# Performance work log

Hardware: AMD Instinct MI355X
Metric: run time of the kernel (lower is better)

## Reference

```python
import jax, jax.numpy as jnp
import numpy as np

B, S, D, H = 4, 4096, 1024, 16
DK = D // H
EPS = 1e-6

def _feature_map(x):
    # ELU + 1 -> strictly positive features
    return jax.nn.elu(x) + 1.0

def setup_inputs() -> dict:
    key = jax.random.key(0)
    ks = jax.random.split(key, 11)
    s = 1.0 / np.sqrt(D)
    return {
        "query": jax.random.normal(ks[0], (B, S, D), jnp.float32),
        "key":   jax.random.normal(ks[1], (B, S, D), jnp.float32),
        "value": jax.random.normal(ks[2], (B, S, D), jnp.float32),
        "Wq": jax.random.uniform(ks[3], (D, D), jnp.float32, -s, s),
        "bq": jax.random.uniform(ks[4], (D,), jnp.float32, -s, s),
        "Wk": jax.random.uniform(ks[5], (D, D), jnp.float32, -s, s),
        "bk": jax.random.uniform(ks[6], (D,), jnp.float32, -s, s),
        "Wv": jax.random.uniform(ks[7], (D, D), jnp.float32, -s, s),
        "bv": jax.random.uniform(ks[8], (D,), jnp.float32, -s, s),
        "Wo": jax.random.uniform(ks[9], (D, D), jnp.float32, -s, s),
        "bo": jax.random.uniform(ks[10], (D,), jnp.float32, -s, s),
    }

def reference(query, key, value, Wq, bq, Wk, bk, Wv, bv, Wo, bo):
    def heads(x, W, b):
        # torch Linear: x @ W.T + b, then split heads -> [B, H, S, DK]
        y = x @ W.T + b
        return y.reshape(B, S, H, DK).transpose(0, 2, 1, 3)

    Q = _feature_map(heads(query, Wq, bq))
    K = _feature_map(heads(key, Wk, bk))
    V = heads(value, Wv, bv)

    # KV[b,h,m,d] = sum_n K[b,h,n,d] * V[b,h,n,m]  (d: K feat dim, m: V dim)
    KV = jnp.einsum('bhnd,bhnm->bhmd', K, V)
    # normalizer Z[b,h,n] = Q[b,h,n,:] . sum_n K
    Z = jnp.einsum('bhnd,bhd->bhn', Q, K.sum(axis=2))[..., None] + EPS
    out = jnp.einsum('bhnd,bhmd->bhnm', Q, KV) / Z  # [B,H,S,DK]
    out = out.transpose(0, 2, 1, 3).reshape(B, S, D)
    return out @ Wo.T + bo
```

## Files before the change

kernel.cpp:

```cpp
#include <hip/hip_runtime.h>
#include <math.h>

#define Bb 4
#define Ss 4096
#define Dd 1024
#define Hh 16
#define DKk 64
#define Mm (Bb * Ss)
#define NCH 16

typedef __attribute__((ext_vector_type(8))) short bf16x8;
typedef __attribute__((ext_vector_type(4))) float f32x4;

__device__ __forceinline__ unsigned short f2bf(float f) {
  unsigned u = __float_as_uint(f);
  u += 0x7FFFu + ((u >> 16) & 1u);
  return (unsigned short)(u >> 16);
}
__device__ __forceinline__ float bf2f(unsigned short s) {
  return __uint_as_float(((unsigned)s) << 16);
}
__device__ __forceinline__ unsigned cvt2(float lo, float hi) {
  unsigned r;
  asm("v_cvt_pk_bf16_f32 %0, %1, %2" : "=v"(r) : "v"(lo), "v"(hi));
  return r;
}
__device__ __forceinline__ void cvt8(const float* __restrict__ s,
                                     unsigned short* __restrict__ d, long i) {
  float4 a = ((const float4*)s)[2 * i];
  float4 b = ((const float4*)s)[2 * i + 1];
  int4 w;
  w.x = cvt2(a.x, a.y); w.y = cvt2(a.z, a.w);
  w.z = cvt2(b.x, b.y); w.w = cvt2(b.z, b.w);
  ((int4*)d)[i] = w;
}

#define GLOAD(dst, src)                                                     \
  __builtin_amdgcn_global_load_lds(                                         \
      (const __attribute__((address_space(1))) void*)(src),                 \
      (__attribute__((address_space(3))) void*)(dst), 16, 0, 0)

__global__ __launch_bounds__(256) void cvt_all(
    const float* __restrict__ k, const float* __restrict__ v,
    const float* __restrict__ Wq, const float* __restrict__ Wk,
    const float* __restrict__ Wv, const float* __restrict__ Wo,
    unsigned short* __restrict__ kb, unsigned short* __restrict__ vb,
    unsigned short* __restrict__ Wqb, unsigned short* __restrict__ Wkb,
    unsigned short* __restrict__ Wvb, unsigned short* __restrict__ Wob) {
  const int z = blockIdx.z;
  if (z < 2) {
    const float* s = z ? v : k;
    unsigned short* d = z ? vb : kb;
    const long n8 = ((long)Mm * Dd) / 8;
    for (long i = (long)blockIdx.x * 256 + threadIdx.x; i < n8;
         i += (long)gridDim.x * 256)
      cvt8(s, d, i);
  } else {
    const long n8w = ((long)Dd * Dd) / 8;
    for (long i = (long)blockIdx.x * 256 + threadIdx.x; i < 4 * n8w;
         i += (long)gridDim.x * 256) {
      const int which = (int)(i / n8w);
      const long off = i - (long)which * n8w;
      const float* s = (which == 0) ? Wq : (which == 1) ? Wk
                       : (which == 2) ? Wv : Wo;
      unsigned short* d = (which == 0) ? Wqb : (which == 1) ? Wkb
                          : (which == 2) ? Wvb : Wob;
      cvt8(s, d, off);
    }
  }
}

#define LOADA2(dst, mh)                                                      \
  _Pragma("unroll") for (int mi = 0; mi < 4; ++mi)                           \
    _Pragma("unroll") for (int ks = 0; ks < 2; ++ks)                         \
      dst[mi][ks] = *(const bf16x8*)(bufA +                                  \
          ((mh) * 128 + wm * 64 + mi * 16 + fr) * 64 + (swz_rd ^ (ks * 32)));

#define LOADB2(dst, nh)                                                      \
  _Pragma("unroll") for (int ni = 0; ni < 2; ++ni)                           \
    _Pragma("unroll") for (int ks = 0; ks < 2; ++ks)                         \
      dst[ni][ks] = *(const bf16x8*)(bufB +                                  \
          ((nh) * 128 + wn * 32 + ni * 16 + fr) * 64 + (swz_rd ^ (ks * 32)));

#define MFMAQ2(a_, b_, mh, nh)                                               \
  __builtin_amdgcn_s_setprio(1);                                             \
  _Pragma("unroll") for (int mi = 0; mi < 4; ++mi)                           \
    _Pragma("unroll") for (int ni = 0; ni < 2; ++ni)                         \
      _Pragma("unroll") for (int ks = 0; ks < 2; ++ks)                       \
        acc[(mh) * 4 + mi][(nh) * 2 + ni] =                                  \
            __builtin_amdgcn_mfma_f32_16x16x32_bf16(                         \
                a_[mi][ks], b_[ni][ks],                                      \
                acc[(mh) * 4 + mi][(nh) * 2 + ni], 0, 0, 0);                 \
  __builtin_amdgcn_s_setprio(0);

template <typename OutT>
__device__ __forceinline__ void gemm256_body(
    const unsigned short* __restrict__ A,
    const unsigned short* __restrict__ W,
    const float* __restrict__ bias,
    OutT* __restrict__ C, const int act, const int wg_in,
    unsigned short* lds) {
  const int t = threadIdx.x;
  const int wave = t >> 6, lane = t & 63;
  const int wm = wave >> 2, wn = wave & 3;
  const int fr = lane & 15, fq = lane >> 4;

  const int wg = ((wg_in & 7) << 5) | (wg_in >> 3);
  const int bm = wg >> 2, bn = wg & 3;

  f32x4 acc[8][4];
#pragma unroll
  for (int i = 0; i < 8; ++i)
#pragma unroll
    for (int j = 0; j < 4; ++j) acc[i][j] = (f32x4){0.f, 0.f, 0.f, 0.f};

  const int r = t >> 3;
  const int swz_st = ((t & 7) ^ (r & 7)) << 3;
  const unsigned short* gA[4];
  const unsigned short* gB[4];
#pragma unroll
  for (int l = 0; l < 4; ++l) {
    const int ga_row = (l & 1) * 128 + (l >> 1) * 64 + r;
    const int bb = l * 2 + (r >> 5);
    const int gb_row = (bb & 3) * 64 + (bb >> 2) * 32 + (r & 31);
    gA[l] = A + (size_t)(bm * 256 + ga_row) * Dd + swz_st;
    gB[l] = W + (size_t)(bn * 256 + gb_row) * Dd + swz_st;
  }
  const int dstoff = wave * 512;

  const int swz_rd = (fq * 8) ^ ((fr & 7) << 3);

  GLOAD(lds + 0 * 4096 + dstoff, gA[0]);
  GLOAD(lds + 1 * 4096 + dstoff, gA[1]);
  GLOAD(lds + 16384 + 0 * 4096 + dstoff, gB[0]);
  GLOAD(lds + 16384 + 1 * 4096 + dstoff, gB[1]);
  GLOAD(lds + 2 * 4096 + dstoff, gA[2]);
  GLOAD(lds + 3 * 4096 + dstoff, gA[3]);
  GLOAD(lds + 16384 + 2 * 4096 + dstoff, gB[2]);
  GLOAD(lds + 16384 + 3 * 4096 + dstoff, gB[3]);
  asm volatile("s_waitcnt vmcnt(4)" ::: "memory");
  __builtin_amdgcn_s_barrier();

  for (int tt = 0; tt < 16; ++tt) {
    unsigned short* bufA = lds + (tt & 1) * 32768;
    unsigned short* bufB = bufA + 16384;
    unsigned short* nA = lds + ((tt & 1) ^ 1) * 32768;
    unsigned short* nB = nA + 16384;
    const int kpre = (tt < 15 ? tt + 1 : 15) * 64;

    bf16x8 afr0[4][2], afr1[4][2], bvr0[2][2], bvr1[2][2];
    LOADA2(afr0, 0)
    LOADB2(bvr0, 0)
    GLOAD(nA + 0 * 4096 + dstoff, gA[0] + kpre);
    GLOAD(nA + 1 * 4096 + dstoff, gA[1] + kpre);
    GLOAD(nB + 0 * 4096 + dstoff, gB[0] + kpre);
    GLOAD(nB + 1 * 4096 + dstoff, gB[1] + kpre);
    asm volatile("s_waitcnt vmcnt(4)" ::: "memory");
    __builtin_amdgcn_s_barrier();
    MFMAQ2(afr0, bvr0, 0, 0)
    LOADB2(bvr1, 1)
    GLOAD(nA + 2 * 4096 + dstoff, gA[2] + kpre);
    GLOAD(nA + 3 * 4096 + dstoff, gA[3] + kpre);
    GLOAD(nB + 2 * 4096 + dstoff, gB[2] + kpre);
    GLOAD(nB + 3 * 4096 + dstoff, gB[3] + kpre);
    MFMAQ2(afr0, bvr1, 0, 1)
    LOADA2(afr1, 1)
    MFMAQ2(afr1, bvr1, 1, 1)
    MFMAQ2(afr1, bvr0, 1, 0)
    asm volatile("s_waitcnt vmcnt(4) lgkmcnt(0)" ::: "memory");
    __builtin_amdgcn_s_barrier();
  }

  const size_t row0 = (size_t)bm * 256 + wm * 128 + fq * 4;
  const int col0 = bn * 256 + wn * 64 + fr;
#pragma unroll
  for (int a = 0; a < 8; ++a) {
    const size_t row_a = row0 + (a >> 2) * 64 + (a & 3) * 16;
#pragma unroll
    for (int b = 0; b < 4; ++b) {
      const int col = col0 + (b >> 1) * 32 + (b & 1) * 16;
      const float bvl = bias[col];
#pragma unroll
      for (int rr2 = 0; rr2 < 4; ++rr2) {
        const size_t row = row_a + rr2;
        float vv = acc[a][b][rr2] + bvl;
        if (act) vv = (vv > 0.f) ? (vv + 1.f) : __expf(vv);
        if constexpr (sizeof(OutT) == 2)
          ((unsigned short*)C)[row * Dd + col] = f2bf(vv);
        else
          ((float*)C)[row * Dd + col] = vv;
      }
    }
  }
}

template <int ACT, typename OutT>
__global__ __launch_bounds__(512, 2) void gemm256(
    const unsigned short* __restrict__ A, const unsigned short* __restrict__ W,
    const float* __restrict__ bias, OutT* __restrict__ C) {
  __shared__ __align__(16) unsigned short lds[2 * 32768];
  gemm256_body<OutT>(A, W, bias, C, ACT,
                     blockIdx.x + gridDim.x * blockIdx.y, lds);
}

__global__ __launch_bounds__(512, 2) void gemm256_kv(
    const unsigned short* __restrict__ A0, const unsigned short* __restrict__ W0,
    const float* __restrict__ b0, unsigned short* __restrict__ C0,
    const unsigned short* __restrict__ A1, const unsigned short* __restrict__ W1,
    const float* __restrict__ b1, unsigned short* __restrict__ C1) {
  __shared__ __align__(16) unsigned short lds[2 * 32768];
  const int wg = blockIdx.x + gridDim.x * blockIdx.y;
  if (blockIdx.z == 0)
    gemm256_body<unsigned short>(A0, W0, b0, C0, 1, wg, lds);
  else
    gemm256_body<unsigned short>(A1, W1, b1, C1, 0, wg, lds);
}

__global__ __launch_bounds__(512, 2) void gemm256_qred(
    const unsigned short* __restrict__ A, const unsigned short* __restrict__ W,
    const float* __restrict__ bias, unsigned short* __restrict__ C,
    const float* __restrict__ part, float* __restrict__ KV,
    float* __restrict__ Ksum) {
  __shared__ __align__(16) unsigned short lds[2 * 32768];
  const int wg = blockIdx.x + gridDim.x * blockIdx.y;
  if (blockIdx.z == 0) {
    gemm256_body<unsigned short>(A, W, bias, C, 1, wg, lds);
  } else {
    const int bh = wg;
    if (bh >= Bb * Hh || threadIdx.x >= 256) return;
    for (int e = threadIdx.x; e < 4160; e += 256) {
      float s = 0.f;
#pragma unroll
      for (int c = 0; c < NCH; ++c)
        s += part[((size_t)bh * NCH + c) * 4160 + e];
      if (e < 4096) KV[(size_t)bh * 4096 + e] = s;
      else Ksum[bh * 64 + (e - 4096)] = s;
    }
  }
}

__global__ __launch_bounds__(256) void kvp_cvtq(
    const unsigned short* __restrict__ Kf, const unsigned short* __restrict__ Vf,
    float* __restrict__ part,
    const float* __restrict__ q, unsigned short* __restrict__ qb) {
  if (blockIdx.y == 1) {
    const long n8 = ((long)Mm * Dd) / 8;
    for (long i = (long)blockIdx.x * 256 + threadIdx.x; i < n8;
         i += (long)gridDim.x * 256)
      cvt8(q, qb, i);
    return;
  }
  const int bx = blockIdx.x;
  if (bx >= Bb * Hh * NCH) return;
  const int chunk = bx % NCH;
  const int bh = bx / NCH;
  const int h = bh % Hh, b = bh / Hh;
  const int t = threadIdx.x;
  const int tm = t >> 4, td = t & 15;
  __shared__ float sK[8][64];
  __shared__ float sV[8][64];
  float acc[4][4] = {{0.f}};
  float ksr[4] = {0.f, 0.f, 0.f, 0.f};

  const int which = t >> 7;
  const int idx = t & 127;
  const int rr = idx >> 4;
  const int dpos = (idx & 15) << 2;
  const int colbase = h * DKk;
  const int rows = Ss / NCH;

  for (int n0 = 0; n0 < rows; n0 += 8) {
    const int gr = b * Ss + chunk * rows + n0 + rr;
    const unsigned short* src = which ? Vf : Kf;
    ushort4 raw = *(const ushort4*)&src[(size_t)gr * Dd + colbase + dpos];
    __syncthreads();
    float* dst = which ? &sV[rr][dpos] : &sK[rr][dpos];
    dst[0] = bf2f(raw.x); dst[1] = bf2f(raw.y);
    dst[2] = bf2f(raw.z); dst[3] = bf2f(raw.w);
    __syncthreads();
#pragma unroll
    for (int r = 0; r < 8; ++r) {
      float kv[4], vv[4];
#pragma unroll
      for (int j = 0; j < 4; ++j) kv[j] = sK[r][td * 4 + j];
#pragma unroll
      for (int i = 0; i < 4; ++i) vv[i] = sV[r][tm * 4 + i];
#pragma unroll
      for (int i = 0; i < 4; ++i)
#pragma unroll
        for (int j = 0; j < 4; ++j)
          acc[i][j] = fmaf(vv[i], kv[j], acc[i][j]);
      if (tm == 0) {
#pragma unroll
        for (int j = 0; j < 4; ++j) ksr[j] += kv[j];
      }
    }
  }

  float* p = part + (size_t)bx * 4160;
#pragma unroll
  for (int i = 0; i < 4; ++i)
#pragma unroll
    for (int j = 0; j < 4; ++j)
      p[(tm * 4 + i) * 64 + td * 4 + j] = acc[i][j];
  if (tm == 0) {
#pragma unroll
    for (int j = 0; j < 4; ++j) p[4096 + td * 4 + j] = ksr[j];
  }
}

__global__ __launch_bounds__(256) void attn_mfma(
    unsigned short* __restrict__ Qf, const float* __restrict__ KV,
    const float* __restrict__ Ksum) {
  const int bh = blockIdx.x;
  const int h = bh & (Hh - 1), b = bh >> 4;
  const int t = threadIdx.x;
  const int wave = t >> 6, lane = t & 63;
  const int fr = lane & 15, fq = lane >> 4;

  bf16x8 bfrag[4][2];
  const float* kvb = KV + (size_t)bh * 4096;
#pragma unroll
  for (int nj = 0; nj < 4; ++nj)
#pragma unroll
    for (int ks = 0; ks < 2; ++ks) {
      const float* src = kvb + (nj * 16 + fr) * 64 + ks * 32 + fq * 8;
      const float4 lo = *(const float4*)src;
      const float4 hi = *(const float4*)(src + 4);
      bf16x8 f;
      f[0] = (short)f2bf(lo.x); f[1] = (short)f2bf(lo.y);
      f[2] = (short)f2bf(lo.z); f[3] = (short)f2bf(lo.w);
      f[4] = (short)f2bf(hi.x); f[5] = (short)f2bf(hi.y);
      f[6] = (short)f2bf(hi.z); f[7] = (short)f2bf(hi.w);
      bfrag[nj][ks] = f;
    }
  bf16x8 zfrag[2];
#pragma unroll
  for (int ks = 0; ks < 2; ++ks) {
    bf16x8 f = (bf16x8){0, 0, 0, 0, 0, 0, 0, 0};
    if (fr == 0) {
      const float* src = Ksum + bh * 64 + ks * 32 + fq * 8;
      const float4 lo = *(const float4*)src;
      const float4 hi = *(const float4*)(src + 4);
      f[0] = (short)f2bf(lo.x); f[1] = (short)f2bf(lo.y);
      f[2] = (short)f2bf(lo.z); f[3] = (short)f2bf(lo.w);
      f[4] = (short)f2bf(hi.x); f[5] = (short)f2bf(hi.y);
      f[6] = (short)f2bf(hi.z); f[7] = (short)f2bf(hi.w);
    }
    zfrag[ks] = f;
  }

  const size_t row0 = (size_t)b * Ss + (size_t)blockIdx.y * 256 + wave * 64;
  unsigned short* qbase = Qf + row0 * Dd + h * DKk;
  bf16x8 afrag[4][2];
#pragma unroll
  for (int mi = 0; mi < 4; ++mi)
#pragma unroll
    for (int ks = 0; ks < 2; ++ks)
      afrag[mi][ks] =
          *(const bf16x8*)(qbase + (size_t)(mi * 16 + fr) * Dd + ks * 32 + fq * 8);

  f32x4 acc[4][4], zacc[4];
#pragma unroll
  for (int mi = 0; mi < 4; ++mi) {
    zacc[mi] = (f32x4){0.f, 0.f, 0.f, 0.f};
#pragma unroll
    for (int nj = 0; nj < 4; ++nj) acc[mi][nj] = (f32x4){0.f, 0.f, 0.f, 0.f};
  }
#pragma unroll
  for (int mi = 0; mi < 4; ++mi)
#pragma unroll
    for (int ks = 0; ks < 2; ++ks) {
      zacc[mi] = __builtin_amdgcn_mfma_f32_16x16x32_bf16(
          afrag[mi][ks], zfrag[ks], zacc[mi], 0, 0, 0);
#pragma unroll
      for (int nj = 0; nj < 4; ++nj)
        acc[mi][nj] = __builtin_amdgcn_mfma_f32_16x16x32_bf16(
            afrag[mi][ks], bfrag[nj][ks], acc[mi][nj], 0, 0, 0);
    }

#pragma unroll
  for (int mi = 0; mi < 4; ++mi)
#pragma unroll
    for (int r = 0; r < 4; ++r) {
      const float zv = __shfl(zacc[mi][r], lane & 48) + 1e-6f;
      const float rz = 1.0f / zv;
      const size_t ro = (size_t)(mi * 16 + fq * 4 + r) * Dd;
#pragma unroll
      for (int nj = 0; nj < 4; ++nj)
        qbase[ro + nj * 16 + fr] = f2bf(acc[mi][nj][r] * rz);
    }
}

extern "C" void kernel_launch(void* const* d_in, const int* in_sizes, int n_in,
                              void* d_out, int out_size, void* d_ws, size_t ws_size,
                              hipStream_t stream) {
  const float* q  = (const float*)d_in[0];
  const float* k  = (const float*)d_in[1];
  const float* v  = (const float*)d_in[2];
  const float* Wq = (const float*)d_in[3];
  const float* bq = (const float*)d_in[4];
  const float* Wk = (const float*)d_in[5];
  const float* bk = (const float*)d_in[6];
  const float* Wv = (const float*)d_in[7];
  const float* bv = (const float*)d_in[8];
  const float* Wo = (const float*)d_in[9];
  const float* bo = (const float*)d_in[10];
  float* out = (float*)d_out;

  unsigned short* kb  = (unsigned short*)d_ws;
  unsigned short* vb  = kb + (size_t)Mm * Dd;
  unsigned short* Kf  = vb + (size_t)Mm * Dd;
  unsigned short* Vf  = Kf + (size_t)Mm * Dd;
  unsigned short* Wqb = Vf + (size_t)Mm * Dd;
  unsigned short* Wkb = Wqb + (size_t)Dd * Dd;
  unsigned short* Wvb = Wkb + (size_t)Dd * Dd;
  unsigned short* Wob = Wvb + (size_t)Dd * Dd;
  float* KV   = (float*)(Wob + (size_t)Dd * Dd);
  float* Ksum = KV + (size_t)Bb * Hh * DKk * DKk;
  float* part = (float*)vb;

  dim3 gg(Dd / 256, Mm / 256);
  dim3 ggz(Dd / 256, Mm / 256, 2);

  cvt_all<<<dim3(2048, 1, 3), 256, 0, stream>>>(k, v, Wq, Wk, Wv, Wo,
                                                kb, vb, Wqb, Wkb, Wvb, Wob);
  gemm256_kv<<<ggz, 512, 0, stream>>>(kb, Wkb, bk, Kf, vb, Wvb, bv, Vf);
  kvp_cvtq<<<dim3(2048, 2), 256, 0, stream>>>(Kf, Vf, part, q, kb);
  gemm256_qred<<<ggz, 512, 0, stream>>>(kb, Wqb, bq, Kf, part, KV, Ksum);
  attn_mfma<<<dim3(Bb * Hh, Ss / 256), 256, 0, stream>>>(Kf, KV, Ksum);
  gemm256<0, float><<<gg, 512, 0, stream>>>(Kf, Wob, bo, out);
  (void)in_sizes; (void)n_in; (void)out_size; (void)ws_size;
}
```

Measured before the change: 262.9 us.

## Load weight fragments directly from global memory into registers, skipping LDS staging

The GEMM body now reads the B operand (weight rows) straight from global memory into MFMA register fragments instead of staging it through LDS, and prefetches the next K-step's B fragment one tile ahead. The loop is unrolled by two so two fragment buffers can ping-pong. LDS use is halved to A tiles only, which lowers LDS traffic and may allow more occupancy. In exchange, each wave issues uncoalesced 16-byte global loads for its weight rows, and the same weight data is fetched redundantly by every wave with the same wn, relying on L2/L1 hits.

```diff
diff --git a/kernel.cpp b/kernel.cpp
--- a/kernel.cpp
+++ b/kernel.cpp
@@ -76,11 +76,11 @@
       dst[mi][ks] = *(const bf16x8*)(bufA +                                  \
           ((mh) * 128 + wm * 64 + mi * 16 + fr) * 64 + (swz_rd ^ (ks * 32)));
 
-#define LOADB2(dst, nh)                                                      \
+#define BLOAD(dst, nh, tt)                                                   \
   _Pragma("unroll") for (int ni = 0; ni < 2; ++ni)                           \
     _Pragma("unroll") for (int ks = 0; ks < 2; ++ks)                         \
-      dst[ni][ks] = *(const bf16x8*)(bufB +                                  \
-          ((nh) * 128 + wn * 32 + ni * 16 + fr) * 64 + (swz_rd ^ (ks * 32)));
+      dst[ni][ks] = *(const bf16x8*)(Wp +                                    \
+          (size_t)((nh) * 32 + ni * 16) * Dd + (tt) * 64 + ks * 32);
 
 #define MFMAQ2(a_, b_, mh, nh)                                               \
   __builtin_amdgcn_s_setprio(1);                                             \
@@ -92,6 +92,29 @@
                 a_[mi][ks], b_[ni][ks],                                      \
                 acc[(mh) * 4 + mi][(nh) * 2 + ni], 0, 0, 0);                 \
   __builtin_amdgcn_s_setprio(0);
+
+#define TILEBODY(tt, B0C, B0N)                                               \
+  {                                                                          \
+    const int kpre = ((tt) < 15 ? (tt) + 1 : 15) * 64;                       \
+    unsigned short* bufA = lds + ((tt) & 1) * 16384;                         \
+    unsigned short* nA = lds + ((((tt) & 1)) ^ 1) * 16384;                   \
+    bf16x8 afr0[4][2], afr1[4][2], B1[2][2];                                 \
+    BLOAD(B1, 1, tt)                                                         \
+    GLOAD(nA + 0 * 4096 + dstoff, gA[0] + kpre);                             \
+    GLOAD(nA + 1 * 4096 + dstoff, gA[1] + kpre);                             \
+    GLOAD(nA + 2 * 4096 + dstoff, gA[2] + kpre);                             \
+    GLOAD(nA + 3 * 4096 + dstoff, gA[3] + kpre);                             \
+    __builtin_amdgcn_sched_barrier(0);                                       \
+    LOADA2(afr0, 0)                                                          \
+    MFMAQ2(afr0, B0C, 0, 0)                                                  \
+    MFMAQ2(afr0, B1, 0, 1)                                                   \
+    LOADA2(afr1, 1)                                                          \
+    MFMAQ2(afr1, B1, 1, 1)                                                   \
+    BLOAD(B0N, 0, ((tt) < 15 ? (tt) + 1 : 15))                               \
+    MFMAQ2(afr1, B0C, 1, 0)                                                  \
+    asm volatile("s_waitcnt vmcnt(4) lgkmcnt(0)" ::: "memory");              \
+    __builtin_amdgcn_s_barrier();                                            \
+  }
 
 template <typename OutT>
 __device__ __forceinline__ void gemm256_body(
@@ -117,58 +140,29 @@
   const int r = t >> 3;
   const int swz_st = ((t & 7) ^ (r & 7)) << 3;
   const unsigned short* gA[4];
-  const unsigned short* gB[4];
 #pragma unroll
   for (int l = 0; l < 4; ++l) {
     const int ga_row = (l & 1) * 128 + (l >> 1) * 64 + r;
-    const int bb = l * 2 + (r >> 5);
-    const int gb_row = (bb & 3) * 64 + (bb >> 2) * 32 + (r & 31);
     gA[l] = A + (size_t)(bm * 256 + ga_row) * Dd + swz_st;
-    gB[l] = W + (size_t)(bn * 256 + gb_row) * Dd + swz_st;
   }
   const int dstoff = wave * 512;
 
   const int swz_rd = (fq * 8) ^ ((fr & 7) << 3);
 
+  const unsigned short* Wp = W + (size_t)(bn * 256 + wn * 64 + fr) * Dd + fq * 8;
+
+  bf16x8 B0a[2][2], B0b[2][2];
   GLOAD(lds + 0 * 4096 + dstoff, gA[0]);
   GLOAD(lds + 1 * 4096 + dstoff, gA[1]);
-  GLOAD(lds + 16384 + 0 * 4096 + dstoff, gB[0]);
-  GLOAD(lds + 16384 + 1 * 4096 + dstoff, gB[1]);
   GLOAD(lds + 2 * 4096 + dstoff, gA[2]);
   GLOAD(lds + 3 * 4096 + dstoff, gA[3]);
-  GLOAD(lds + 16384 + 2 * 4096 + dstoff, gB[2]);
-  GLOAD(lds + 16384 + 3 * 4096 + dstoff, gB[3]);
-  asm volatile("s_waitcnt vmcnt(4)" ::: "memory");
+  BLOAD(B0a, 0, 0)
+  asm volatile("s_waitcnt vmcnt(0)" ::: "memory");
   __builtin_amdgcn_s_barrier();
 
-  for (int tt = 0; tt < 16; ++tt) {
-    unsigned short* bufA = lds + (tt & 1) * 32768;
-    unsigned short* bufB = bufA + 16384;
-    unsigned short* nA = lds + ((tt & 1) ^ 1) * 32768;
-    unsigned short* nB = nA + 16384;
-    const int kpre = (tt < 15 ? tt + 1 : 15) * 64;
-
-    bf16x8 afr0[4][2], afr1[4][2], bvr0[2][2], bvr1[2][2];
-    LOADA2(afr0, 0)
-    LOADB2(bvr0, 0)
-    GLOAD(nA + 0 * 4096 + dstoff, gA[0] + kpre);
-    GLOAD(nA + 1 * 4096 + dstoff, gA[1] + kpre);
-    GLOAD(nB + 0 * 4096 + dstoff, gB[0] + kpre);
-    GLOAD(nB + 1 * 4096 + dstoff, gB[1] + kpre);
-    asm volatile("s_waitcnt vmcnt(4)" ::: "memory");
-    __builtin_amdgcn_s_barrier();
-    MFMAQ2(afr0, bvr0, 0, 0)
-    LOADB2(bvr1, 1)
-    GLOAD(nA + 2 * 4096 + dstoff, gA[2] + kpre);
-    GLOAD(nA + 3 * 4096 + dstoff, gA[3] + kpre);
-    GLOAD(nB + 2 * 4096 + dstoff, gB[2] + kpre);
-    GLOAD(nB + 3 * 4096 + dstoff, gB[3] + kpre);
-    MFMAQ2(afr0, bvr1, 0, 1)
-    LOADA2(afr1, 1)
-    MFMAQ2(afr1, bvr1, 1, 1)
-    MFMAQ2(afr1, bvr0, 1, 0)
-    asm volatile("s_waitcnt vmcnt(4) lgkmcnt(0)" ::: "memory");
-    __builtin_amdgcn_s_barrier();
+  for (int th = 0; th < 8; ++th) {
+    TILEBODY(2 * th, B0a, B0b)
+    TILEBODY(2 * th + 1, B0b, B0a)
   }
 
   const size_t row0 = (size_t)bm * 256 + wm * 128 + fq * 4;
@@ -198,7 +192,7 @@
 __global__ __launch_bounds__(512, 2) void gemm256(
     const unsigned short* __restrict__ A, const unsigned short* __restrict__ W,
     const float* __restrict__ bias, OutT* __restrict__ C) {
-  __shared__ __align__(16) unsigned short lds[2 * 32768];
+  __shared__ __align__(16) unsigned short lds[2 * 16384];
   gemm256_body<OutT>(A, W, bias, C, ACT,
                      blockIdx.x + gridDim.x * blockIdx.y, lds);
 }
@@ -208,7 +202,7 @@
     const float* __restrict__ b0, unsigned short* __restrict__ C0,
     const unsigned short* __restrict__ A1, const unsigned short* __restrict__ W1,
     const float* __restrict__ b1, unsigned short* __restrict__ C1) {
-  __shared__ __align__(16) unsigned short lds[2 * 32768];
+  __shared__ __align__(16) unsigned short lds[2 * 16384];
   const int wg = blockIdx.x + gridDim.x * blockIdx.y;
   if (blockIdx.z == 0)
     gemm256_body<unsigned short>(A0, W0, b0, C0, 1, wg, lds);
@@ -221,7 +215,7 @@
     const float* __restrict__ bias, unsigned short* __restrict__ C,
     const float* __restrict__ part, float* __restrict__ KV,
     float* __restrict__ Ksum) {
-  __shared__ __align__(16) unsigned short lds[2 * 32768];
+  __shared__ __align__(16) unsigned short lds[2 * 16384];
   const int wg = blockIdx.x + gridDim.x * blockIdx.y;
   if (blockIdx.z == 0) {
     gemm256_body<unsigned short>(A, W, bias, C, 1, wg, lds);
```

New measurement: 309.3 us. 1.18x slower.
